# Kernel tuning notes

Measured on AMD Instinct MI355X. Metric: run time of the kernel, lower is better.

The kernel has to match this reference:

```python
import jax, jax.numpy as jnp
import numpy as np
from jax import lax

N, C, F, W = 4096, 1, 15, 120
STRIDE = 10
NW = W // STRIDE            # 12 windows
P = F * (F - 1) // 2        # 105 pairs
HP = 2 * P + 4 * F          # 270 stacked stat rows
FC1_IN = 16 * HP * (NW - 2) # 43200
FC2, FC3, FCAST = 512, 128, 1
BN_EPS = 1e-5

# static pair indices, same order as generate(list(range(F)))
_II, _JJ = np.triu_indices(F, k=1)


def _fill(x):
    # numpy_fill: replace nan/inf with 0
    return jnp.where(jnp.isfinite(x), x, jnp.zeros_like(x))


def setup_inputs() -> dict:
    key = jax.random.key(0)
    ks = jax.random.split(key, 13)
    inp = {
        'data': jax.random.uniform(ks[0], (N, C, F, W), dtype=jnp.float32),
        'bn_gamma': jax.random.normal(ks[1], (C,), dtype=jnp.float32),
        'bn_beta': jax.random.normal(ks[2], (C,), dtype=jnp.float32),
        'bn_mean': jax.random.normal(ks[3], (C,), dtype=jnp.float32) * 0.1,
        'bn_var': jax.random.uniform(ks[4], (C,), dtype=jnp.float32) + 0.5,
        'conv_w': jax.random.normal(ks[5], (16, 1, 1, 3), dtype=jnp.float32) * 0.1,
        'conv_b': jax.random.normal(ks[6], (16,), dtype=jnp.float32) * 0.1,
        'fc1_w': jax.random.normal(ks[7], (FC2, FC1_IN), dtype=jnp.float32) * (1.0 / np.sqrt(FC1_IN)),
        'fc1_b': jax.random.normal(ks[8], (FC2,), dtype=jnp.float32) * 0.01,
        'fc2_w': jax.random.normal(ks[9], (FC3, FC2), dtype=jnp.float32) * (1.0 / np.sqrt(FC2)),
        'fc2_b': jax.random.normal(ks[10], (FC3,), dtype=jnp.float32) * 0.01,
        'fc3_w': jax.random.normal(ks[11], (FCAST, FC3), dtype=jnp.float32) * (1.0 / np.sqrt(FC3)),
        'fc3_b': jax.random.normal(ks[12], (FCAST,), dtype=jnp.float32) * 0.01,
    }
    return inp


def _features(data):
    # data: [N,C,F,W] -> windows [N,C,F,NW,S]
    S = STRIDE
    win = data.reshape(data.shape[0], data.shape[1], F, NW, S)
    mean = win.mean(axis=-1)                         # [N,C,F,NW]
    spread = win - mean[..., None]
    var_u = (spread * spread).sum(axis=-1) / (S - 1)  # unbiased, matches torch .std()
    std = jnp.sqrt(var_u)
    # pairwise cov / corr over (II, JJ)
    cov = (spread[:, :, _II] * spread[:, :, _JJ]).sum(axis=-1) / (S - 1)  # [N,C,P,NW]
    corr = _fill(cov / (std[:, :, _II] * std[:, :, _JJ]) * ((S - 1) / S))
    cov = _fill(cov)
    stdf = _fill(std)
    zs = _fill(mean / std)
    ret = _fill(win[..., -1] / win[..., 0] - 1.0)
    w = jnp.arange(1, S + 1, dtype=jnp.float32)
    w = w / w.sum()
    dl = _fill((win * w).sum(axis=-1))
    # concat along feature rows, order as in forward: corr,cov,std,zscore,return,decaylinear
    return jnp.concatenate([corr, cov, stdf, zs, ret, dl], axis=2)  # [N,C,HP,NW]


def reference(data, bn_gamma, bn_beta, bn_mean, bn_var, conv_w, conv_b,
              fc1_w, fc1_b, fc2_w, fc2_b, fc3_w, fc3_b):
    feat = _features(data)  # [N,1,HP,NW]
    # BatchNorm2d (eval mode, running stats)
    x = (feat - bn_mean[None, :, None, None]) * lax.rsqrt(bn_var + BN_EPS)[None, :, None, None]
    x = x * bn_gamma[None, :, None, None] + bn_beta[None, :, None, None]
    # Conv2d(1,16,(1,3)) valid padding
    x = lax.conv_general_dilated(x, conv_w, window_strides=(1, 1), padding='VALID',
                                 dimension_numbers=('NCHW', 'OIHW', 'NCHW'))
    x = jax.nn.relu(x + conv_b[None, :, None, None])  # [N,16,HP,NW-2]
    x = x.reshape(x.shape[0], -1)                      # [N, FC1_IN]
    # MLP head (dropout = identity in eval)
    x = jax.nn.relu(x @ fc1_w.T + fc1_b)
    x = jax.nn.sigmoid(x @ fc2_w.T + fc2_b)
    out = (x @ fc3_w.T + fc3_b)[:, 0]                  # fc3(...).T[0] -> [N]
    return out
```

## Files before the change

### kernel.cpp

```cpp
#include <hip/hip_runtime.h>
#include <cstdint>
#include <cstddef>


typedef _Float16 f16;
typedef f16 f16x8 __attribute__((ext_vector_type(8)));
typedef float f32x4 __attribute__((ext_vector_type(4)));

#define CHUNK   2048
#define K_FC1   43200
#define KT_TOT  675
#define TILE_F  16384
#define HALF_F  8192

__device__ __forceinline__ float fillv(float x) { return isfinite(x) ? x : 0.0f; }

__global__ __launch_bounds__(256) void retile_w(const float* __restrict__ w,
                                                f16* __restrict__ Wt) {
    const int bid = blockIdx.x;
    const int nt = bid / KT_TOT, kt = bid % KT_TOT;
    const int t = threadIdx.x;
    f16* dst = Wt + (size_t)bid * TILE_F;
    #pragma unroll
    for (int j = 0; j < 8; ++j) {
        int q = t + 256 * j;
        int half = q >> 10, rr = (q >> 3) & 127, c = q & 7;
        const float* s = w + (size_t)(nt * 256 + half * 128 + rr) * K_FC1 + kt * 64 + c * 8;
        float4 x = *(const float4*)s;
        float4 y = *(const float4*)(s + 4);
        f16x8 o = { (f16)x.x, (f16)x.y, (f16)x.z, (f16)x.w,
                    (f16)y.x, (f16)y.y, (f16)y.z, (f16)y.w };
        int p = c ^ (rr & 7);
        *(f16x8*)(dst + (size_t)half * HALF_F + rr * 64 + p * 8) = o;
    }
}

__global__ __launch_bounds__(256) void stage_a(
    const float* __restrict__ data, const float* __restrict__ bn_g,
    const float* __restrict__ bn_b, const float* __restrict__ bn_m,
    const float* __restrict__ bn_v, const float* __restrict__ conv_w,
    const float* __restrict__ conv_b, f16* __restrict__ A16, int n0)
{
    __shared__ float raw[1800];
    __shared__ float feat[270 * 12];
    __shared__ float cw[48];
    __shared__ float cb[16];
    __shared__ int   pi[105], pj[105];

    const int t = threadIdx.x;
    const int n = n0 + blockIdx.x;
    const float4* src4 = (const float4*)(data + (size_t)n * 1800);
    for (int i = t; i < 450; i += 256) ((float4*)raw)[i] = src4[i];
    if (t < 48)  cw[t] = conv_w[t];
    if (t < 16)  cb[t] = conv_b[t];
    if (t < 105) {
        int i = 0, rem = t;
        while (rem >= 14 - i) { rem -= 14 - i; ++i; }
        pi[t] = i; pj[t] = i + 1 + rem;
    }
    __syncthreads();

    if (t < 180) {
        int f = t / 12, w = t % 12;
        int base = f * 120 + w * 10;
        float x[10];
        #pragma unroll
        for (int s = 0; s < 10; ++s) x[s] = raw[base + s];
        float sum = 0.f;
        #pragma unroll
        for (int s = 0; s < 10; ++s) sum += x[s];
        float mean = sum * 0.1f;
        float ret = x[9] / x[0] - 1.0f;
        float dl = 0.f;
        #pragma unroll
        for (int s = 0; s < 10; ++s) dl += x[s] * ((float)(s + 1) * (1.0f / 55.0f));
        float var = 0.f;
        #pragma unroll
        for (int s = 0; s < 10; ++s) { float d = x[s] - mean; raw[base + s] = d; var += d * d; }
        var *= (1.0f / 9.0f);
        float sd = sqrtf(var);
        feat[(210 + f) * 12 + w] = fillv(sd);
        feat[(225 + f) * 12 + w] = fillv(mean / sd);
        feat[(240 + f) * 12 + w] = fillv(ret);
        feat[(255 + f) * 12 + w] = fillv(dl);
    }
    __syncthreads();

    for (int q = t; q < 1260; q += 256) {
        int p = q / 12, w = q % 12;
        int i = pi[p], j = pj[p];
        int bi = i * 120 + w * 10, bj = j * 120 + w * 10;
        float cv = 0.f;
        #pragma unroll
        for (int s = 0; s < 10; ++s) cv += raw[bi + s] * raw[bj + s];
        cv *= (1.0f / 9.0f);
        float si = feat[(210 + i) * 12 + w], sj = feat[(210 + j) * 12 + w];
        feat[p * 12 + w]         = fillv(cv / (si * sj) * 0.9f);
        feat[(105 + p) * 12 + w] = fillv(cv);
    }
    __syncthreads();

    float a  = bn_g[0] * rsqrtf(bn_v[0] + 1e-5f);
    float bb = bn_b[0] - bn_m[0] * a;
    for (int i = t; i < 3240; i += 256) feat[i] = feat[i] * a + bb;
    __syncthreads();

    const int s_idx = blockIdx.x;
    const int mt = s_idx >> 8, r256 = s_idx & 255;
    const int half = r256 >> 7, rloc = r256 & 127, rsw = r256 & 7;
    f16* abase = A16 + ((size_t)(mt * KT_TOT) * 2 + half) * HALF_F + (size_t)rloc * 64;
    for (int v = t; v < K_FC1 / 8; v += 256) {
        int idx0 = v * 8;
        f16x8 ov;
        #pragma unroll
        for (int e = 0; e < 8; ++e) {
            int idx = idx0 + e;
            int oc = idx / 2700;
            int rem = idx - oc * 2700;
            int h = rem / 10;
            int wo = rem - h * 10;
            const float* fr = feat + h * 12 + wo;
            float y = cb[oc] + cw[oc * 3] * fr[0] + cw[oc * 3 + 1] * fr[1] + cw[oc * 3 + 2] * fr[2];
            y = y > 0.f ? y : 0.f;
            y *= 0.00390625f;
            y = y < 65000.f ? y : 65000.f;
            ov[e] = (f16)y;
        }
        int kt = v >> 3, c = v & 7;
        int p = c ^ rsw;
        *(f16x8*)(abase + (size_t)kt * TILE_F + p * 8) = ov;
    }
}

__global__ __launch_bounds__(512, 2) void gemm_fc1(const f16* __restrict__ A,
                                                   const f16* __restrict__ W,
                                                   float* __restrict__ Ysum)
{
    extern __shared__ f16 lds[];

    const int bid = blockIdx.x;
    const int mt = bid & 7;
    const int slot = bid >> 3;
    const int nt = slot & 1;
    const int sk = slot >> 1;
    const int kt0 = sk * 42 + (sk < 3 ? sk : 3);
    const int cnt = 42 + (sk < 3 ? 1 : 0);

    const int tid = threadIdx.x;
    const int wave = tid >> 6, lane = tid & 63;
    const int quad = lane >> 4, m16 = lane & 15;
    const int rsw = m16 & 7;
    const int wm = (wave & 1) << 6;
    const int wn = (wave >> 1) << 5;

    const f16* Ab = A + (size_t)(mt * KT_TOT + kt0) * TILE_F;
    const f16* Bb = W + (size_t)(nt * KT_TOT + kt0) * TILE_F;

    f32x4 acc[8][4] = {};
    f16x8 a[4][2], bA[2][2], bB[2][2];

#define STAGE_A(BUF, HALF, KI) do {                                            \
    const f16* g_ = Ab + (size_t)(KI) * TILE_F + (HALF) * HALF_F + tid * 8;    \
    f16* l_ = lds + (BUF) * TILE_F + (HALF) * HALF_F + tid * 8;                \
    __builtin_amdgcn_global_load_lds(                                          \
        (const __attribute__((address_space(1))) void*)g_,                     \
        (__attribute__((address_space(3))) void*)l_, 16, 0, 0);                \
    __builtin_amdgcn_global_load_lds(                                          \
        (const __attribute__((address_space(1))) void*)(g_ + 4096),            \
        (__attribute__((address_space(3))) void*)(l_ + 4096), 16, 0, 0);       \
} while (0)

#define STAGE_B(BUF, HALF, KI) do {                                            \
    const f16* g_ = Bb + (size_t)(KI) * TILE_F + (HALF) * HALF_F + tid * 8;    \
    f16* l_ = lds + 32768 + (BUF) * TILE_F + (HALF) * HALF_F + tid * 8;        \
    __builtin_amdgcn_global_load_lds(                                          \
        (const __attribute__((address_space(1))) void*)g_,                     \
        (__attribute__((address_space(3))) void*)l_, 16, 0, 0);                \
    __builtin_amdgcn_global_load_lds(                                          \
        (const __attribute__((address_space(1))) void*)(g_ + 4096),            \
        (__attribute__((address_space(3))) void*)(l_ + 4096), 16, 0, 0);       \
} while (0)

#define RD_A(MH, BUF) do {                                                     \
    _Pragma("unroll") for (int i2_ = 0; i2_ < 4; ++i2_)                        \
    _Pragma("unroll") for (int kh_ = 0; kh_ < 2; ++kh_)                        \
        a[i2_][kh_] = *(const f16x8*)(lds + (BUF) * TILE_F + (MH) * HALF_F     \
            + (wm + i2_ * 16 + m16) * 64 + (((kh_ * 4 + quad) ^ rsw) << 3));   \
} while (0)

#define RD_B(DST, NH, BUF) do {                                                \
    _Pragma("unroll") for (int j2_ = 0; j2_ < 2; ++j2_)                        \
    _Pragma("unroll") for (int kh_ = 0; kh_ < 2; ++kh_)                        \
        DST[j2_][kh_] = *(const f16x8*)(lds + 32768 + (BUF) * TILE_F           \
            + (NH) * HALF_F                                                    \
            + (wn + j2_ * 16 + m16) * 64 + (((kh_ * 4 + quad) ^ rsw) << 3));   \
} while (0)

#define MMA(IO, JO, BF) do {                                                   \
    _Pragma("unroll") for (int i2_ = 0; i2_ < 4; ++i2_)                        \
    _Pragma("unroll") for (int j2_ = 0; j2_ < 2; ++j2_)                        \
    _Pragma("unroll") for (int kh_ = 0; kh_ < 2; ++kh_)                        \
        acc[(IO) + i2_][(JO) + j2_] = __builtin_amdgcn_mfma_f32_16x16x32_f16(  \
            a[i2_][kh_], BF[j2_][kh_], acc[(IO) + i2_][(JO) + j2_], 0, 0, 0);  \
} while (0)

    STAGE_A(0, 0, 0);
    STAGE_B(0, 0, 0);
    STAGE_B(0, 1, 0);
    STAGE_A(0, 1, 0);
    asm volatile("s_waitcnt vmcnt(4)" ::: "memory");
    __builtin_amdgcn_s_barrier();

    #pragma unroll 1
    for (int ti = 0; ti < cnt - 1; ++ti) {
        const int bc = ti & 1, bn = bc ^ 1;
        RD_A(0, bc); RD_B(bA, 0, bc);
        STAGE_A(bn, 0, ti + 1);
        __builtin_amdgcn_s_barrier();
        __builtin_amdgcn_s_setprio(1);
        MMA(0, 0, bA);
        __builtin_amdgcn_s_setprio(0);
        asm volatile("s_waitcnt vmcnt(4)" ::: "memory");
        __builtin_amdgcn_s_barrier();
        RD_B(bB, 1, bc);
        STAGE_B(bn, 0, ti + 1);
        __builtin_amdgcn_s_barrier();
        __builtin_amdgcn_s_setprio(1);
        MMA(0, 2, bB);
        __builtin_amdgcn_s_setprio(0);
        asm volatile("s_waitcnt vmcnt(4)" ::: "memory");
        __builtin_amdgcn_s_barrier();
        RD_A(1, bc);
        STAGE_B(bn, 1, ti + 1);
        __builtin_amdgcn_s_barrier();
        __builtin_amdgcn_s_setprio(1);
        MMA(4, 2, bB);
        __builtin_amdgcn_s_setprio(0);
        __builtin_amdgcn_s_barrier();
        STAGE_A(bn, 1, ti + 1);
        __builtin_amdgcn_s_barrier();
        __builtin_amdgcn_s_setprio(1);
        MMA(4, 0, bA);
        __builtin_amdgcn_s_setprio(0);
        asm volatile("s_waitcnt vmcnt(4)" ::: "memory");
        __builtin_amdgcn_s_barrier();
    }

    {
        const int bc = (cnt - 1) & 1;
        RD_A(0, bc); RD_B(bA, 0, bc);
        __builtin_amdgcn_s_setprio(1);
        MMA(0, 0, bA);
        __builtin_amdgcn_s_setprio(0);
        asm volatile("s_waitcnt vmcnt(2)" ::: "memory");
        __builtin_amdgcn_s_barrier();
        RD_B(bB, 1, bc);
        __builtin_amdgcn_s_setprio(1);
        MMA(0, 2, bB);
        __builtin_amdgcn_s_setprio(0);
        asm volatile("s_waitcnt vmcnt(0)" ::: "memory");
        __builtin_amdgcn_s_barrier();
        RD_A(1, bc);
        __builtin_amdgcn_s_setprio(1);
        MMA(4, 2, bB);
        MMA(4, 0, bA);
        __builtin_amdgcn_s_setprio(0);
    }

#undef STAGE_A
#undef STAGE_B
#undef RD_A
#undef RD_B
#undef MMA

    float* Yb = Ysum + (size_t)(mt * 256) * 512 + nt * 256;
    #pragma unroll
    for (int i = 0; i < 8; ++i) {
        const int row0 = (i >> 2) * 128 + wm + (i & 3) * 16 + quad * 4;
        #pragma unroll
        for (int j = 0; j < 4; ++j) {
            const int col = (j >> 1) * 128 + wn + (j & 1) * 16 + m16;
            #pragma unroll
            for (int r = 0; r < 4; ++r)
                unsafeAtomicAdd(&Yb[(size_t)(row0 + r) * 512 + col], acc[i][j][r]);
        }
    }
}

__global__ __launch_bounds__(128) void head_fc23(const float* __restrict__ y1s,
                                                 const float* __restrict__ b1,
                                                 const float* __restrict__ w2,
                                                 const float* __restrict__ b2,
                                                 const float* __restrict__ w3,
                                                 const float* __restrict__ b3,
                                                 float* __restrict__ out, int n0)
{
    __shared__ float Ys[8 * 512];
    __shared__ float Y2[8 * 128];
    const int t = threadIdx.x;
    const float4* yb = (const float4*)(y1s + (size_t)blockIdx.x * 8 * 512);
    const float4* b1v = (const float4*)b1;
    for (int i = t; i < 8 * 128; i += 128) {
        float4 s = yb[i];
        float4 bv = b1v[i & 127];
        float4 y;
        y.x = fmaxf(fmaf(s.x, 256.f, bv.x), 0.f);
        y.y = fmaxf(fmaf(s.y, 256.f, bv.y), 0.f);
        y.z = fmaxf(fmaf(s.z, 256.f, bv.z), 0.f);
        y.w = fmaxf(fmaf(s.w, 256.f, bv.w), 0.f);
        ((float4*)Ys)[i] = y;
    }
    __syncthreads();

    float acc[8];
    float bk = b2[t];
    #pragma unroll
    for (int s = 0; s < 8; ++s) acc[s] = bk;
    const float4* wr = (const float4*)(w2 + (size_t)t * 512);
    for (int jc = 0; jc < 128; ++jc) {
        float4 w4 = wr[jc];
        #pragma unroll
        for (int s = 0; s < 8; ++s) {
            float4 y4 = *(const float4*)(Ys + s * 512 + jc * 4);
            acc[s] += w4.x * y4.x + w4.y * y4.y + w4.z * y4.z + w4.w * y4.w;
        }
    }
    #pragma unroll
    for (int s = 0; s < 8; ++s) Y2[s * 128 + t] = 1.0f / (1.0f + expf(-acc[s]));
    __syncthreads();

    if (t < 8) {
        float sm = b3[0];
        #pragma unroll 4
        for (int k = 0; k < 128; ++k) sm += Y2[t * 128 + k] * w3[k];
        out[n0 + blockIdx.x * 8 + t] = sm;
    }
}

extern "C" void kernel_launch(void* const* d_in, const int* in_sizes, int n_in,
                              void* d_out, int out_size, void* d_ws, size_t ws_size,
                              hipStream_t stream)
{
    const float* data = (const float*)d_in[0];
    const float* bn_g = (const float*)d_in[1];
    const float* bn_b = (const float*)d_in[2];
    const float* bn_m = (const float*)d_in[3];
    const float* bn_v = (const float*)d_in[4];
    const float* cw   = (const float*)d_in[5];
    const float* cb   = (const float*)d_in[6];
    const float* fc1w = (const float*)d_in[7];
    const float* fc1b = (const float*)d_in[8];
    const float* fc2w = (const float*)d_in[9];
    const float* fc2b = (const float*)d_in[10];
    const float* fc3w = (const float*)d_in[11];
    const float* fc3b = (const float*)d_in[12];
    float* out = (float*)d_out;

    const size_t A16_BYTES = (size_t)CHUNK * K_FC1 * 2;
    const size_t W16_BYTES = (size_t)512 * K_FC1 * 2;
    const size_t Y1_BYTES  = (size_t)CHUNK * 512 * 4;
    if (ws_size < A16_BYTES + W16_BYTES + Y1_BYTES) return;

    char* ws = (char*)d_ws;
    f16*   A16 = (f16*)ws;
    f16*   W16 = (f16*)(ws + A16_BYTES);
    float* y1s = (float*)(ws + A16_BYTES + W16_BYTES);

    static int smem_set = 0;
    if (!smem_set) {
        hipFuncSetAttribute(reinterpret_cast<const void*>(gemm_fc1),
                            hipFuncAttributeMaxDynamicSharedMemorySize, 131072);
        smem_set = 1;
    }

    retile_w<<<2 * KT_TOT, 256, 0, stream>>>(fc1w, W16);

    for (int c = 0; c < 2; ++c) {
        int n0 = c * CHUNK;
        hipMemsetAsync(y1s, 0, Y1_BYTES, stream);
        stage_a<<<CHUNK, 256, 0, stream>>>(data, bn_g, bn_b, bn_m, bn_v, cw, cb, A16, n0);
        gemm_fc1<<<256, 512, 131072, stream>>>(A16, W16, y1s);
        head_fc23<<<CHUNK / 8, 128, 0, stream>>>(y1s, fc1b, fc2w, fc2b, fc3w, fc3b, out, n0);
    }
}
```

Baseline: 597.7 us.

## Fold batchnorm into conv weights and stage conv output through LDS

The eval-mode batchnorm affine is folded into the conv weights and bias, which removes a full pass over the feature buffer and one barrier. The conv+relu epilogue is restructured so each thread computes a whole 10-wide row for one output channel from vectorized float4 feature loads. Results are staged in shared memory as f16 in four channel groups, then written out as contiguous swizzled 16-byte stores. LDS reads for the window stats and covariance are also widened to float2. The staging adds extra barriers and reuses the raw-data buffer as scratch.

```diff
diff --git a/kernel.cpp b/kernel.cpp
--- a/kernel.cpp
+++ b/kernel.cpp
@@ -4,6 +4,7 @@
 
 
 typedef _Float16 f16;
+typedef f16 f16x2 __attribute__((ext_vector_type(2)));
 typedef f16 f16x8 __attribute__((ext_vector_type(8)));
 typedef float f32x4 __attribute__((ext_vector_type(4)));
 
@@ -41,18 +42,26 @@
     const float* __restrict__ bn_v, const float* __restrict__ conv_w,
     const float* __restrict__ conv_b, f16* __restrict__ A16, int n0)
 {
-    __shared__ float raw[1800];
-    __shared__ float feat[270 * 12];
-    __shared__ float cw[48];
-    __shared__ float cb[16];
+    __shared__ __align__(16) float pool[5400];
+    __shared__ __align__(16) float feat[270 * 12];
+    __shared__ float cwf[48];
+    __shared__ float cbf[16];
     __shared__ int   pi[105], pj[105];
+
+    float* raw = pool;
+    f16*   cstage = (f16*)pool;
 
     const int t = threadIdx.x;
     const int n = n0 + blockIdx.x;
     const float4* src4 = (const float4*)(data + (size_t)n * 1800);
-    for (int i = t; i < 450; i += 256) ((float4*)raw)[i] = src4[i];
-    if (t < 48)  cw[t] = conv_w[t];
-    if (t < 16)  cb[t] = conv_b[t];
+    for (int i = t; i < 450; i += 256) ((float4*)pool)[i] = src4[i];
+
+    {
+        float a  = bn_g[0] * rsqrtf(bn_v[0] + 1e-5f);
+        float bb = bn_b[0] - bn_m[0] * a;
+        if (t < 48) cwf[t] = conv_w[t] * a;
+        if (t < 16) cbf[t] = conv_b[t] + bb * (conv_w[3 * t] + conv_w[3 * t + 1] + conv_w[3 * t + 2]);
+    }
     if (t < 105) {
         int i = 0, rem = t;
         while (rem >= 14 - i) { rem -= 14 - i; ++i; }
@@ -63,9 +72,9 @@
     if (t < 180) {
         int f = t / 12, w = t % 12;
         int base = f * 120 + w * 10;
-        float x[10];
-        #pragma unroll
-        for (int s = 0; s < 10; ++s) x[s] = raw[base + s];
+        const float2* r2 = (const float2*)(raw + base);
+        float2 p0 = r2[0], p1 = r2[1], p2 = r2[2], p3 = r2[3], p4 = r2[4];
+        float x[10] = { p0.x, p0.y, p1.x, p1.y, p2.x, p2.y, p3.x, p3.y, p4.x, p4.y };
         float sum = 0.f;
         #pragma unroll
         for (int s = 0; s < 10; ++s) sum += x[s];
@@ -75,8 +84,12 @@
         #pragma unroll
         for (int s = 0; s < 10; ++s) dl += x[s] * ((float)(s + 1) * (1.0f / 55.0f));
         float var = 0.f;
-        #pragma unroll
-        for (int s = 0; s < 10; ++s) { float d = x[s] - mean; raw[base + s] = d; var += d * d; }
+        float d[10];
+        #pragma unroll
+        for (int s = 0; s < 10; ++s) { d[s] = x[s] - mean; var += d[s] * d[s]; }
+        float2* w2p = (float2*)(raw + base);
+        #pragma unroll
+        for (int s = 0; s < 5; ++s) w2p[s] = make_float2(d[2 * s], d[2 * s + 1]);
         var *= (1.0f / 9.0f);
         float sd = sqrtf(var);
         feat[(210 + f) * 12 + w] = fillv(sd);
@@ -89,10 +102,14 @@
     for (int q = t; q < 1260; q += 256) {
         int p = q / 12, w = q % 12;
         int i = pi[p], j = pj[p];
-        int bi = i * 120 + w * 10, bj = j * 120 + w * 10;
+        const float2* ri = (const float2*)(raw + i * 120 + w * 10);
+        const float2* rj = (const float2*)(raw + j * 120 + w * 10);
         float cv = 0.f;
         #pragma unroll
-        for (int s = 0; s < 10; ++s) cv += raw[bi + s] * raw[bj + s];
+        for (int s = 0; s < 5; ++s) {
+            float2 ai = ri[s], aj = rj[s];
+            cv += ai.x * aj.x + ai.y * aj.y;
+        }
         cv *= (1.0f / 9.0f);
         float si = feat[(210 + i) * 12 + w], sj = feat[(210 + j) * 12 + w];
         feat[p * 12 + w]         = fillv(cv / (si * sj) * 0.9f);
@@ -100,35 +117,47 @@
     }
     __syncthreads();
 
-    float a  = bn_g[0] * rsqrtf(bn_v[0] + 1e-5f);
-    float bb = bn_b[0] - bn_m[0] * a;
-    for (int i = t; i < 3240; i += 256) feat[i] = feat[i] * a + bb;
-    __syncthreads();
-
     const int s_idx = blockIdx.x;
     const int mt = s_idx >> 8, r256 = s_idx & 255;
     const int half = r256 >> 7, rloc = r256 & 127, rsw = r256 & 7;
     f16* abase = A16 + ((size_t)(mt * KT_TOT) * 2 + half) * HALF_F + (size_t)rloc * 64;
-    for (int v = t; v < K_FC1 / 8; v += 256) {
-        int idx0 = v * 8;
-        f16x8 ov;
-        #pragma unroll
-        for (int e = 0; e < 8; ++e) {
-            int idx = idx0 + e;
-            int oc = idx / 2700;
-            int rem = idx - oc * 2700;
-            int h = rem / 10;
-            int wo = rem - h * 10;
-            const float* fr = feat + h * 12 + wo;
-            float y = cb[oc] + cw[oc * 3] * fr[0] + cw[oc * 3 + 1] * fr[1] + cw[oc * 3 + 2] * fr[2];
-            y = y > 0.f ? y : 0.f;
-            y *= 0.00390625f;
-            y = y < 65000.f ? y : 65000.f;
-            ov[e] = (f16)y;
+
+    for (int p = 0; p < 4; ++p) {
+        #pragma unroll
+        for (int j = 0; j < 5; ++j) {
+            int item = t + (j << 8);
+            if (item < 1080) {
+                int h = item >> 2, ocl = item & 3, oc = (p << 2) + ocl;
+                const float4* f4 = (const float4*)(feat + h * 12);
+                float4 fa = f4[0], fb = f4[1], fc = f4[2];
+                float fv[12] = { fa.x, fa.y, fa.z, fa.w,
+                                 fb.x, fb.y, fb.z, fb.w,
+                                 fc.x, fc.y, fc.z, fc.w };
+                float w0 = cwf[oc * 3], w1 = cwf[oc * 3 + 1], w2 = cwf[oc * 3 + 2];
+                float bz = cbf[oc];
+                int kl = ocl * 2700 + h * 10;
+                #pragma unroll
+                for (int q = 0; q < 5; ++q) {
+                    float y0 = fmaf(w2, fv[2 * q + 2], fmaf(w1, fv[2 * q + 1], fmaf(w0, fv[2 * q], bz)));
+                    float y1 = fmaf(w2, fv[2 * q + 3], fmaf(w1, fv[2 * q + 2], fmaf(w0, fv[2 * q + 1], bz)));
+                    y0 = fminf(fmaxf(y0, 0.f) * 0.00390625f, 65000.f);
+                    y1 = fminf(fmaxf(y1, 0.f) * 0.00390625f, 65000.f);
+                    *(f16x2*)(cstage + kl + 2 * q) = f16x2{ (f16)y0, (f16)y1 };
+                }
+            }
         }
-        int kt = v >> 3, c = v & 7;
-        int p = c ^ rsw;
-        *(f16x8*)(abase + (size_t)kt * TILE_F + p * 8) = ov;
+        __syncthreads();
+        #pragma unroll
+        for (int j = 0; j < 6; ++j) {
+            int u = t + (j << 8);
+            if (u < 1350) {
+                int U = p * 1350 + u;
+                int kt = U >> 3, c = U & 7;
+                f16x8 ov = *(const f16x8*)(cstage + u * 8);
+                *(f16x8*)(abase + (size_t)kt * TILE_F + ((c ^ rsw) << 3)) = ov;
+            }
+        }
+        __syncthreads();
     }
 }
 
```

Result: faster. 545.1 us (-8.8%).
